# Performance work log

Hardware: AMD Instinct MI355X
Metric: run time of the kernel (lower is better)

## Reference

```python
import jax, jax.numpy as jnp
import numpy as np
import math

B, S, HID = 4, 2048, 1024
H, D = 16, HID // 16


def setup_inputs() -> dict:
    key = jax.random.key(0)
    ks = jax.random.split(key, 6)
    scale = 0.02
    inp = {
        "hidden_states": jax.random.normal(ks[0], (B, S, HID), dtype=jnp.float32),
        "Wq": jax.random.normal(ks[1], (HID, HID), dtype=jnp.float32) * scale,
        "bq": jnp.zeros((HID,), dtype=jnp.float32),
        "Wk1": jax.random.normal(ks[2], (HID, HID), dtype=jnp.float32) * scale,
        "bk1": jnp.zeros((HID,), dtype=jnp.float32),
        "Wk2": jax.random.normal(ks[3], (HID, HID), dtype=jnp.float32) * scale,
        "bk2": jnp.zeros((HID,), dtype=jnp.float32),
        "Wv1": jax.random.normal(ks[4], (HID, HID), dtype=jnp.float32) * scale,
        "bv1": jnp.zeros((HID,), dtype=jnp.float32),
        "Wv2": jax.random.normal(ks[5], (HID, HID), dtype=jnp.float32) * scale,
        "bv2": jnp.zeros((HID,), dtype=jnp.float32),
    }
    return inp


def _heads(x):
    # [B, S, HID] -> [B, H, S, D]
    return x.reshape(B, S, H, D).transpose(0, 2, 1, 3)


def reference(hidden_states, Wq, bq, Wk1, bk1, Wk2, bk2, Wv1, bv1, Wv2, bv2):
    # nn.Linear uses y = x @ W^T + b
    q = _heads(hidden_states @ Wq.T + bq)
    k1 = _heads(hidden_states @ Wk1.T + bk1)
    k2 = _heads(hidden_states @ Wk2.T + bk2)
    v1 = _heads(hidden_states @ Wv1.T + bv1)
    v2 = _heads(hidden_states @ Wv2.T + bv2)

    inv_sqrt_d = 1.0 / math.sqrt(D)
    scores = jnp.einsum('bhqd,bhkd->bhqk', q, k1) * inv_sqrt_d  # [B,H,S,S]
    probs = jax.nn.softmax(scores, axis=-1)
    ctx = jnp.einsum('bhqk,bhkd->bhqd', probs, v1)              # [B,H,S,D]
    ctx = jnp.einsum('bhqd,bhkd->bhqk', ctx, k2)                # [B,H,S,S]
    ctx = jnp.einsum('bhqk,bhkd->bhqd', ctx, v2)                # [B,H,S,D]
    # [B,H,S,D] -> [B,S,HID]
    return ctx.transpose(0, 2, 1, 3).reshape(B, S, HID)
```

## Files before the change

kernel.cpp:

```cpp
#include <hip/hip_runtime.h>
#include <hip/hip_bf16.h>

#define HIDD 1024
#define BATCH 4
#define SEQ 2048
#define NHEAD 16
#define HD 64
#define NW 5
#define MROWS (BATCH*SEQ)
#define NCOLS (NW*HIDD)

typedef __attribute__((ext_vector_type(8))) short bf16x8;
typedef __attribute__((ext_vector_type(4))) float f32x4;
typedef __attribute__((ext_vector_type(16))) float f32x16;
typedef __attribute__((ext_vector_type(4))) unsigned int uint4v;

__device__ __forceinline__ unsigned short f2b(float f) {
    __hip_bfloat16 h = __float2bfloat16(f);
    return __builtin_bit_cast(unsigned short, h);
}
__device__ __forceinline__ float b2f(unsigned short u) {
    __hip_bfloat16 h = __builtin_bit_cast(__hip_bfloat16, u);
    return __bfloat162float(h);
}

#if __has_builtin(__builtin_amdgcn_exp2f)
#define EXP2(x) __builtin_amdgcn_exp2f(x)
#else
#define EXP2(x) exp2f(x)
#endif

typedef __attribute__((address_space(1))) const void gvoid;
typedef __attribute__((address_space(3))) void lvoid;
__device__ __forceinline__ void gload16(const void* src, void* dst) {
    __builtin_amdgcn_global_load_lds((gvoid*)src, (lvoid*)dst, 16, 0, 0);
}

__global__ void cvt_kernel(const float* __restrict__ X,
                           const float* __restrict__ W0, const float* __restrict__ W1,
                           const float* __restrict__ W2, const float* __restrict__ W3,
                           const float* __restrict__ W4,
                           unsigned short* __restrict__ Xb, unsigned short* __restrict__ Wb)
{
    const int XN = MROWS * HIDD / 4;
    const int WN = HIDD * HIDD / 4;
    int i = blockIdx.x * 256 + threadIdx.x;
    if (i >= XN + 5 * WN) return;
    const float* src; unsigned short* dst; int off;
    if (i < XN) { src = X; dst = Xb; off = i; }
    else {
        int j = i - XN; int w = j / WN; int r = j - w * WN;
        src = (w == 0 ? W0 : w == 1 ? W1 : w == 2 ? W2 : w == 3 ? W3 : W4);
        dst = Wb + (long)w * HIDD * HIDD; off = r;
    }
    float4 v = ((const float4*)src)[off];
    short4 o;
    o.x = (short)f2b(v.x); o.y = (short)f2b(v.y);
    o.z = (short)f2b(v.z); o.w = (short)f2b(v.w);
    ((short4*)dst)[off] = o;
}

#define READ_A(buf, kh, mh) \
    _Pragma("unroll") \
    for (int mt = 0; mt < 4; ++mt) \
        af[mt] = *(const bf16x8*)((const char*)As[buf][kh] + \
                  (wr * 128 + (mh) * 64 + mt * 16 + q) * 64 + ((g ^ csw) << 4));
#define READ_B(buf, kh) \
    _Pragma("unroll") \
    for (int nt = 0; nt < 4; ++nt) \
        bfr[nt] = *(const bf16x8*)((const char*)Bs[buf][kh] + \
                  (wc * 64 + nt * 16 + q) * 64 + ((g ^ csw) << 4));
#define MFMA_Q(mh) \
    asm volatile("s_waitcnt lgkmcnt(0)" ::: "memory"); \
    __builtin_amdgcn_sched_barrier(0); \
    __builtin_amdgcn_s_setprio(1); \
    _Pragma("unroll") \
    for (int mt = 0; mt < 4; ++mt) \
    _Pragma("unroll") \
    for (int nt = 0; nt < 4; ++nt) \
        acc[(mh) * 4 + mt][nt] = __builtin_amdgcn_mfma_f32_16x16x32_bf16( \
            af[mt], bfr[nt], acc[(mh) * 4 + mt][nt], 0, 0, 0); \
    __builtin_amdgcn_s_setprio(0);

__global__ __launch_bounds__(512, 2) void gemm_proj(
    const unsigned short* __restrict__ Xb, const unsigned short* __restrict__ Wb,
    const float* __restrict__ pb0, const float* __restrict__ pb1, const float* __restrict__ pb2,
    const float* __restrict__ pb3, const float* __restrict__ pb4,
    unsigned short* __restrict__ C)
{
    __shared__ __align__(16) unsigned short As[2][2][256 * 32];
    __shared__ __align__(16) unsigned short Bs[2][2][256 * 32];
    int tid = threadIdx.x;
    int n = blockIdx.x;
    int xcd = n & 7, o = n >> 3;
    int bm = xcd * 4 + (o & 3);
    int bn = o >> 2;
    int lane = tid & 63, w = tid >> 6;
    int wr = w >> 2, wc = w & 3;
    int q = lane & 15, g = lane >> 4;
    int csw = (q >> 1) & 3;

    f32x4 acc[8][4] = {};

    const unsigned short* Ag = Xb + (long)(bm * 256) * HIDD;
    const unsigned short* Bg = Wb + (long)(bn * 256) * HIDD;
    int srow = tid >> 2;
    int scol = ((tid & 3) ^ ((tid >> 3) & 3)) * 8;

    auto stage = [&](const unsigned short* G, unsigned short* slot, int kc) {
#pragma unroll
        for (int l = 0; l < 2; ++l)
            gload16(G + (long)(l * 128 + srow) * HIDD + kc + scol,
                    (char*)slot + (l * 512 + tid) * 16);
    };

    stage(Ag, As[0][0], 0);
    stage(Bg, Bs[0][0], 0);
    stage(Ag, As[0][1], 32);
    stage(Bg, Bs[0][1], 32);
    stage(Ag, As[1][0], 64);
    stage(Bg, Bs[1][0], 64);

    for (int t = 0; t < 16; ++t) {
        int buf = t & 1;
        int kc1 = ((t + 1) & 15) * 64;
        int kc2 = ((t + 2) & 15) * 64;
        bf16x8 af[4], bfr[4];
        asm volatile("s_waitcnt vmcnt(8)" ::: "memory");
        asm volatile("s_barrier" ::: "memory");
        READ_A(buf, 0, 0)
        READ_B(buf, 0)
        stage(Ag, As[buf ^ 1][1], kc1 + 32);
        MFMA_Q(0)
        READ_A(buf, 0, 1)
        stage(Bg, Bs[buf ^ 1][1], kc1 + 32);
        MFMA_Q(1)
        asm volatile("s_waitcnt vmcnt(8)" ::: "memory");
        asm volatile("s_barrier" ::: "memory");
        READ_A(buf, 1, 0)
        READ_B(buf, 1)
        stage(Ag, As[buf][0], kc2);
        MFMA_Q(0)
        READ_A(buf, 1, 1)
        stage(Bg, Bs[buf][0], kc2);
        MFMA_Q(1)
    }

    int ncol0 = bn * 256 + wc * 64 + q;
    const float* bp = (bn < 4 ? pb0 : bn < 8 ? pb1 : bn < 12 ? pb2 : bn < 16 ? pb3 : pb4);
#pragma unroll
    for (int nt = 0; nt < 4; ++nt) {
        int ncol = ncol0 + nt * 16;
        float bv = bp[ncol & 1023];
#pragma unroll
        for (int mt = 0; mt < 8; ++mt) {
            int row = bm * 256 + wr * 128 + mt * 16 + g * 4;
#pragma unroll
            for (int r = 0; r < 4; ++r)
                C[(long)(row + r) * NCOLS + ncol] = f2b(acc[mt][nt][r] + bv);
        }
    }
}

#define QSCALE 0.180336880f
#define LDV 72
#define NT (SEQ / 64)

__global__ __launch_bounds__(256, 4) void flash1(
    const unsigned short* __restrict__ C, unsigned short* __restrict__ ctx)
{
    __shared__ unsigned short Ks[2][64 * 64];
    __shared__ unsigned short Vs[2][64 * LDV];
    __shared__ float Lbuf[4][32];
    int tid = threadIdx.x;
    int lane = tid & 63, w = tid >> 6;
    int q32 = lane & 31, hi = lane >> 5;
    int n = blockIdx.x;
    int qt = (n >> 3) & 15;
    int bh = (n & 7) * 8 + (n >> 7);
    int b = bh >> 4, h = bh & 15;
    long rowbase = (long)(b * SEQ) * NCOLS;
    int s0 = qt * 128;

    const unsigned short* Kg = C + rowbase + 1 * HIDD + h * 64;
    const unsigned short* Vg = C + rowbase + 3 * HIDD + h * 64;

    int krlo = lane >> 3;
    int kch  = (lane & 7) ^ krlo;
    int kp = tid & 31, dc = tid >> 5;
    int rsw = q32 & 7;

    bf16x8 qreg[4];
    {
        const unsigned short* Qp = C + rowbase + (long)(s0 + w * 32 + q32) * NCOLS + h * 64;
#pragma unroll
        for (int s = 0; s < 4; ++s) {
            bf16x8 v = *(const bf16x8*)(Qp + s * 16 + hi * 8);
#pragma unroll
            for (int j = 0; j < 8; j++)
                v[j] = (short)f2b(b2f((unsigned short)v[j]) * QSCALE);
            qreg[s] = v;
        }
    }

#pragma unroll
    for (int t = 0; t < 2; ++t) {
        int li = t * 4 + w;
        gload16(Kg + (long)(li * 8 + krlo) * NCOLS + kch * 8,
                (char*)Ks[0] + li * 1024 + (lane << 4));
    }
    {
        const unsigned short* vsrc = Vg + (long)(2 * kp) * NCOLS + dc * 8;
        bf16x8 v0 = *(const bf16x8*)vsrc;
        bf16x8 v1 = *(const bf16x8*)(vsrc + NCOLS);
        unsigned int* VsW = (unsigned int*)Vs[0];
#pragma unroll
        for (int j = 0; j < 8; j++) {
            unsigned int pk = ((unsigned int)(unsigned short)v0[j]) |
                              (((unsigned int)(unsigned short)v1[j]) << 16);
            VsW[(dc * 8 + j) * (LDV / 2) + kp] = pk;
        }
    }
    __syncthreads();

    f32x16 O0 = {}, O1 = {};
    float l_run = 0.f;

    auto body = [&](int kt, int cur, int nxt) {
        int ktn = (kt + 1) & (NT - 1);
#pragma unroll
        for (int t = 0; t < 2; ++t) {
            int li = t * 4 + w;
            gload16(Kg + (long)(ktn * 64 + li * 8 + krlo) * NCOLS + kch * 8,
                    (char*)Ks[nxt] + li * 1024 + (lane << 4));
        }
        const unsigned short* nsrc = Vg + (long)(ktn * 64 + 2 * kp) * NCOLS + dc * 8;
        bf16x8 nv0 = *(const bf16x8*)nsrc;
        bf16x8 nv1 = *(const bf16x8*)(nsrc + NCOLS);

        float lsum = 0.f;
        __builtin_amdgcn_s_setprio(1);
#pragma unroll
        for (int kb = 0; kb < 2; ++kb) {
            f32x16 st = {};
#pragma unroll
            for (int s = 0; s < 4; ++s) {
                bf16x8 kf = *(const bf16x8*)((const char*)Ks[cur] +
                             ((kb * 32 + q32) << 7) + (((2 * s + hi) ^ rsw) << 4));
                st = __builtin_amdgcn_mfma_f32_32x32x16_bf16(kf, qreg[s], st, 0, 0, 0);
            }
            float e[16];
#pragma unroll
            for (int r = 0; r < 16; ++r) e[r] = EXP2(st[r]);
            lsum += (((e[0]+e[1])+(e[2]+e[3])) + ((e[4]+e[5])+(e[6]+e[7])))
                  + (((e[8]+e[9])+(e[10]+e[11])) + ((e[12]+e[13])+(e[14]+e[15])));
            unsigned int Cw[8];
#pragma unroll
            for (int p = 0; p < 8; ++p)
                asm("v_cvt_pk_bf16_f32 %0, %1, %2" : "=v"(Cw[p]) : "v"(e[2*p]), "v"(e[2*p+1]));
#pragma unroll
            for (int t2 = 0; t2 < 2; ++t2) {
                unsigned int a0 = Cw[t2*4+0], a1 = Cw[t2*4+1];
                unsigned int a2 = Cw[t2*4+2], a3 = Cw[t2*4+3];
                asm("v_permlane32_swap_b32 %0, %1" : "+v"(a0), "+v"(a2));
                asm("v_permlane32_swap_b32 %0, %1" : "+v"(a1), "+v"(a3));
                uint4v aw; aw[0] = a0; aw[1] = a1; aw[2] = a2; aw[3] = a3;
                bf16x8 af = __builtin_bit_cast(bf16x8, aw);
                int t = kb * 2 + t2;
#pragma unroll
                for (int nt = 0; nt < 2; ++nt) {
                    bf16x8 vf = *(const bf16x8*)((const char*)Vs[cur] +
                                 (nt * 32 + q32) * (LDV * 2) + t * 32 + hi * 16);
                    if (nt == 0) O0 = __builtin_amdgcn_mfma_f32_32x32x16_bf16(af, vf, O0, 0, 0, 0);
                    else         O1 = __builtin_amdgcn_mfma_f32_32x32x16_bf16(af, vf, O1, 0, 0, 0);
                }
            }
        }
        __builtin_amdgcn_s_setprio(0);
        l_run += lsum;
        {
            unsigned int* VsWn = (unsigned int*)Vs[nxt];
#pragma unroll
            for (int j = 0; j < 8; ++j) {
                unsigned int pk = ((unsigned int)(unsigned short)nv0[j]) |
                                  (((unsigned int)(unsigned short)nv1[j]) << 16);
                VsWn[(dc * 8 + j) * (LDV / 2) + kp] = pk;
            }
        }
        __syncthreads();
    };

    for (int kt = 0; kt < NT; kt += 2) {
        body(kt, 0, 1);
        body(kt + 1, 1, 0);
    }

    l_run += __shfl_xor(l_run, 32);
    float linv = 1.f / l_run;
    Lbuf[w][q32] = linv;
    asm volatile("s_waitcnt lgkmcnt(0)" ::: "memory");
#pragma unroll
    for (int reg = 0; reg < 16; ++reg) {
        int row = (reg & 3) + 8 * (reg >> 2) + 4 * hi;
        float lr = Lbuf[w][row];
        unsigned short* dst = ctx + ((long)bh * SEQ + s0 + w * 32 + row) * 64 + q32;
        dst[0]  = f2b(O0[reg] * lr);
        dst[32] = f2b(O1[reg] * lr);
    }
}

#define LDT2 72
__global__ __launch_bounds__(256) void m_partial(
    const unsigned short* __restrict__ C, float* __restrict__ part)
{
    __shared__ unsigned short Kt[64 * LDT2];
    __shared__ unsigned short Vt[64 * LDT2];
    int tid = threadIdx.x;
    int lane = tid & 63, w = tid >> 6;
    int q32 = lane & 31, hi = lane >> 5;
    int sc = blockIdx.x;
    int bh = blockIdx.y; int b = bh >> 4, h = bh & 15;
    const unsigned short* K2 = C + (long)(b * SEQ) * NCOLS + 2 * HIDD + h * 64;
    const unsigned short* V2 = C + (long)(b * SEQ) * NCOLS + 4 * HIDD + h * 64;
    int kp = tid & 31, dc = tid >> 5;
    int d2h = w >> 1, d1h = w & 1;
    unsigned int* KtW = (unsigned int*)Kt;
    unsigned int* VtW = (unsigned int*)Vt;
    f32x16 acc = {};

    for (int tk = 0; tk < 4; ++tk) {
        int sbase = sc * 256 + tk * 64;
        if (tk) __syncthreads();
        const unsigned short* ks = K2 + (long)(sbase + 2 * kp) * NCOLS + dc * 8;
        bf16x8 k0 = *(const bf16x8*)ks, k1 = *(const bf16x8*)(ks + NCOLS);
        const unsigned short* vs = V2 + (long)(sbase + 2 * kp) * NCOLS + dc * 8;
        bf16x8 v0 = *(const bf16x8*)vs, v1 = *(const bf16x8*)(vs + NCOLS);
#pragma unroll
        for (int j = 0; j < 8; ++j) {
            KtW[(dc * 8 + j) * (LDT2 / 2) + kp] =
                (unsigned int)(unsigned short)k0[j] | ((unsigned int)(unsigned short)k1[j] << 16);
            VtW[(dc * 8 + j) * (LDT2 / 2) + kp] =
                (unsigned int)(unsigned short)v0[j] | ((unsigned int)(unsigned short)v1[j] << 16);
        }
        __syncthreads();
#pragma unroll
        for (int t = 0; t < 4; ++t) {
            bf16x8 afr = *(const bf16x8*)(Vt + (d2h * 32 + q32) * LDT2 + t * 16 + hi * 8);
            bf16x8 bfr = *(const bf16x8*)(Kt + (d1h * 32 + q32) * LDT2 + t * 16 + hi * 8);
            acc = __builtin_amdgcn_mfma_f32_32x32x16_bf16(afr, bfr, acc, 0, 0, 0);
        }
    }
    float* dst = part + ((long)(sc * 64 + bh) << 12);
#pragma unroll
    for (int reg = 0; reg < 16; ++reg) {
        int d2 = d2h * 32 + (reg & 3) + 8 * (reg >> 2) + 4 * hi;
        dst[d2 * 64 + d1h * 32 + q32] = acc[reg];
    }
}

__global__ void m_reduce(const float* __restrict__ part, float* __restrict__ MT)
{
    int i = blockIdx.x * 256 + threadIdx.x;
    if (i >= 64 * 4096) return;
    int bh = i >> 12, e = i & 4095;
    float s = 0.f;
#pragma unroll
    for (int sc = 0; sc < 8; sc++) s += part[((long)(sc * 64 + bh) << 12) + e];
    MT[i] = s;
}

#define LDF 72
__global__ __launch_bounds__(256) void final_out(
    const unsigned short* __restrict__ ctx, const float* __restrict__ MT,
    float* __restrict__ out)
{
    __shared__ unsigned short cs[64 * LDF];
    __shared__ float ms[64 * 65];
    int tid = threadIdx.x;
    int st0 = blockIdx.x * 4;
    int bh = blockIdx.y; int b = bh >> 4, h = bh & 15;
    {
        const float* Msrc = MT + ((long)bh << 12);
        for (int i = tid; i < 4096; i += 256) ms[(i >> 6) * 65 + (i & 63)] = Msrc[i];
    }
    int s = tid & 63, d2b = (tid >> 6) * 16;
    for (int ti = 0; ti < 4; ++ti) {
        int st = st0 + ti;
        if (ti) __syncthreads();
        {
            int i = tid >> 2, dcx = tid & 3;
            const unsigned short* src = ctx + ((long)bh * SEQ + st * 64 + i) * 64 + dcx * 16;
            *(int4*)(cs + i * LDF + dcx * 16)     = *(const int4*)src;
            *(int4*)(cs + i * LDF + dcx * 16 + 8) = *(const int4*)(src + 8);
        }
        __syncthreads();
        float acc[16] = {};
        for (int d1 = 0; d1 < 64; d1 += 8) {
            bf16x8 cv = *(const bf16x8*)(cs + s * LDF + d1);
#pragma unroll
            for (int dd = 0; dd < 8; dd++) {
                float c = b2f((unsigned short)cv[dd]);
#pragma unroll
                for (int j = 0; j < 16; j++)
                    acc[j] += c * ms[(d2b + j) * 65 + d1 + dd];
            }
        }
        float* dst = out + (long)(b * SEQ + st * 64 + s) * HIDD + h * 64 + d2b;
#pragma unroll
        for (int j = 0; j < 16; j++) dst[j] = acc[j];
    }
}

extern "C" void kernel_launch(void* const* d_in, const int* in_sizes, int n_in,
                              void* d_out, int out_size, void* d_ws, size_t ws_size,
                              hipStream_t stream)
{
    const float* X   = (const float*)d_in[0];
    const float* Wq  = (const float*)d_in[1];
    const float* bq  = (const float*)d_in[2];
    const float* Wk1 = (const float*)d_in[3];
    const float* bk1 = (const float*)d_in[4];
    const float* Wk2 = (const float*)d_in[5];
    const float* bk2 = (const float*)d_in[6];
    const float* Wv1 = (const float*)d_in[7];
    const float* bv1 = (const float*)d_in[8];
    const float* Wv2 = (const float*)d_in[9];
    const float* bv2 = (const float*)d_in[10];

    char* ws = (char*)d_ws;
    unsigned short* Xb  = (unsigned short*)(ws);
    unsigned short* Wb  = (unsigned short*)(ws + 16777216);
    unsigned short* C   = (unsigned short*)(ws + 27262976);
    unsigned short* ctx = (unsigned short*)(ws + 111149056);
    float* part         = (float*)(ws + 127926272);
    float* MT           = (float*)(ws + 136314880);
    float* out = (float*)d_out;

    cvt_kernel<<<dim3(13312), 256, 0, stream>>>(X, Wq, Wk1, Wk2, Wv1, Wv2, Xb, Wb);
    gemm_proj<<<dim3(640), 512, 0, stream>>>(Xb, Wb, bq, bk1, bk2, bv1, bv2, C);
    flash1<<<dim3(1024), 256, 0, stream>>>(C, ctx);
    m_partial<<<dim3(8, 64), 256, 0, stream>>>(C, part);
    m_reduce<<<dim3(1024), 256, 0, stream>>>(part, MT);
    final_out<<<dim3(8, 64), 256, 0, stream>>>(ctx, MT, out);
}
```

Before: 279.5 us.

## Restructure projection GEMM pipeline to stage next K tile with barrier-bracketed MFMA phases

```diff
diff --git a/kernel.cpp b/kernel.cpp
--- a/kernel.cpp
+++ b/kernel.cpp
@@ -60,17 +60,18 @@
     ((short4*)dst)[off] = o;
 }
 
-#define READ_A(buf, kh, mh) \
+#define READ_A4(buf, kh, mh) \
     _Pragma("unroll") \
     for (int mt = 0; mt < 4; ++mt) \
-        af[mt] = *(const bf16x8*)((const char*)As[buf][kh] + \
+        a[mt] = *(const bf16x8*)((const char*)As[buf][kh] + \
                   (wr * 128 + (mh) * 64 + mt * 16 + q) * 64 + ((g ^ csw) << 4));
-#define READ_B(buf, kh) \
+#define READ_B4(buf, kh) \
     _Pragma("unroll") \
     for (int nt = 0; nt < 4; ++nt) \
-        bfr[nt] = *(const bf16x8*)((const char*)Bs[buf][kh] + \
+        b[nt] = *(const bf16x8*)((const char*)Bs[buf][kh] + \
                   (wc * 64 + nt * 16 + q) * 64 + ((g ^ csw) << 4));
-#define MFMA_Q(mh) \
+#define PHASE_TAIL(mh) \
+    asm volatile("s_barrier" ::: "memory"); \
     asm volatile("s_waitcnt lgkmcnt(0)" ::: "memory"); \
     __builtin_amdgcn_sched_barrier(0); \
     __builtin_amdgcn_s_setprio(1); \
@@ -79,8 +80,9 @@
     _Pragma("unroll") \
     for (int nt = 0; nt < 4; ++nt) \
         acc[(mh) * 4 + mt][nt] = __builtin_amdgcn_mfma_f32_16x16x32_bf16( \
-            af[mt], bfr[nt], acc[(mh) * 4 + mt][nt], 0, 0, 0); \
-    __builtin_amdgcn_s_setprio(0);
+            a[mt], b[nt], acc[(mh) * 4 + mt][nt], 0, 0, 0); \
+    __builtin_amdgcn_s_setprio(0); \
+    asm volatile("s_barrier" ::: "memory");
 
 __global__ __launch_bounds__(512, 2) void gemm_proj(
     const unsigned short* __restrict__ Xb, const unsigned short* __restrict__ Wb,
@@ -118,32 +120,30 @@
     stage(Bg, Bs[0][0], 0);
     stage(Ag, As[0][1], 32);
     stage(Bg, Bs[0][1], 32);
-    stage(Ag, As[1][0], 64);
-    stage(Bg, Bs[1][0], 64);
+    asm volatile("s_waitcnt vmcnt(4)" ::: "memory");
+    asm volatile("s_barrier" ::: "memory");
 
     for (int t = 0; t < 16; ++t) {
         int buf = t & 1;
         int kc1 = ((t + 1) & 15) * 64;
-        int kc2 = ((t + 2) & 15) * 64;
-        bf16x8 af[4], bfr[4];
-        asm volatile("s_waitcnt vmcnt(8)" ::: "memory");
-        asm volatile("s_barrier" ::: "memory");
-        READ_A(buf, 0, 0)
-        READ_B(buf, 0)
+        bf16x8 a[4], b[4];
+
+        READ_B4(buf, 0)
+        READ_A4(buf, 0, 0)
+        stage(Ag, As[buf ^ 1][0], kc1);
+        PHASE_TAIL(0)
+        READ_A4(buf, 0, 1)
+        stage(Bg, Bs[buf ^ 1][0], kc1);
+        asm volatile("s_waitcnt vmcnt(4)" ::: "memory");
+        PHASE_TAIL(1)
+        READ_B4(buf, 1)
+        READ_A4(buf, 1, 0)
         stage(Ag, As[buf ^ 1][1], kc1 + 32);
-        MFMA_Q(0)
-        READ_A(buf, 0, 1)
+        PHASE_TAIL(0)
+        READ_A4(buf, 1, 1)
         stage(Bg, Bs[buf ^ 1][1], kc1 + 32);
-        MFMA_Q(1)
-        asm volatile("s_waitcnt vmcnt(8)" ::: "memory");
-        asm volatile("s_barrier" ::: "memory");
-        READ_A(buf, 1, 0)
-        READ_B(buf, 1)
-        stage(Ag, As[buf][0], kc2);
-        MFMA_Q(0)
-        READ_A(buf, 1, 1)
-        stage(Bg, Bs[buf][0], kc2);
-        MFMA_Q(1)
+        asm volatile("s_waitcnt vmcnt(4)" ::: "memory");
+        PHASE_TAIL(1)
     }
 
     int ncol0 = bn * 256 + wc * 64 + q;
```

Result: slower. 287.4 us (+2.8%).
